# Performance work log

Hardware: AMD Instinct MI355X
Metric: run time of the kernel (lower is better)

## Reference

```python
import jax, jax.numpy as jnp
import numpy as np

N = 50000
E = 800000
HIDDEN = 128
NUM_HEADS = 8
D_HEAD = HIDDEN // NUM_HEADS


def setup_inputs() -> dict:
    key = jax.random.key(0)
    ks = jax.random.split(key, 12)
    sc = 1.0 / np.sqrt(HIDDEN)
    inp = {
        "h": jax.random.normal(ks[0], (N, HIDDEN), dtype=jnp.float32),
        "rows": jax.random.randint(ks[1], (E,), 0, N, dtype=jnp.int32),
        "cols": jax.random.randint(ks[2], (E,), 0, N, dtype=jnp.int32),
        "Wq": jax.random.normal(ks[3], (HIDDEN, HIDDEN), dtype=jnp.float32) * sc,
        "bq": jax.random.normal(ks[4], (HIDDEN,), dtype=jnp.float32) * sc,
        "Wk": jax.random.normal(ks[5], (HIDDEN, HIDDEN), dtype=jnp.float32) * sc,
        "bk": jax.random.normal(ks[6], (HIDDEN,), dtype=jnp.float32) * sc,
        "Wv": jax.random.normal(ks[7], (HIDDEN, HIDDEN), dtype=jnp.float32) * sc,
        "bv": jax.random.normal(ks[8], (HIDDEN,), dtype=jnp.float32) * sc,
        "Wo": jax.random.normal(ks[9], (HIDDEN, HIDDEN), dtype=jnp.float32) * sc,
        "bo": jax.random.normal(ks[10], (HIDDEN,), dtype=jnp.float32) * sc,
    }
    return inp


def reference(h, rows, cols, Wq, bq, Wk, bk, Wv, bv, Wo, bo):
    n = h.shape[0]
    scaling = D_HEAD ** (-0.5)
    # projections; torch-style reshape splits hidden as (d_head, num_heads)
    q = ((h @ Wq.T + bq).reshape(n, D_HEAD, NUM_HEADS)) * scaling
    k = (h @ Wk.T + bk).reshape(n, D_HEAD, NUM_HEADS)
    v = (h @ Wv.T + bv).reshape(n, D_HEAD, NUM_HEADS)
    # SDDMM: per-edge, per-head score = q[row] . k[col]   -> [E, H]
    scores = jnp.einsum("edh,edh->eh", q[rows], k[cols])
    # row-wise (destination) stable softmax over variable-degree neighborhoods
    m = jax.ops.segment_max(scores, rows, num_segments=n)  # [N, H]
    e = jnp.exp(scores - m[rows])
    s = jax.ops.segment_sum(e, rows, num_segments=n)  # [N, H]
    attn = e / s[rows]  # [E, H]
    # SpMM: out[i] = sum_{(i,j) in E} attn[e] * v[j]
    out = jax.ops.segment_sum(attn[:, None, :] * v[cols], rows, num_segments=n)
    return out.reshape(n, HIDDEN) @ Wo.T + bo
```

## Files before the change

kernel.cpp:

```cpp
#include <hip/hip_runtime.h>
#include <math.h>

#define N_NODES 50000
#define N_EDGES 800000
#define HID 128
#define CAP 64

#define SCAT_TH   (N_EDGES / 8)
#define SCAT_BLK  ((SCAT_TH + 255) / 256)
#define WCVT_BLK  64
#define HCVT_BLK  (N_NODES * HID / 4 / 256)
#define PREP_BLK  (SCAT_BLK + WCVT_BLK + HCVT_BLK)

#define QKV_BX    ((N_NODES + 31) / 32)
#define ATTN_BLK  ((N_NODES + 3) / 4)
#define OUT_BLK   ((N_NODES + 63) / 64)

typedef _Float16 f16_t;
typedef f16_t f16x8 __attribute__((ext_vector_type(8)));
typedef f16_t f16x2 __attribute__((ext_vector_type(2)));
typedef float f32x4 __attribute__((ext_vector_type(4)));

__device__ __forceinline__ ushort f2h_bits(float x) {
    union { f16_t h; ushort u; } c; c.h = (f16_t)x; return c.u;
}
__device__ __forceinline__ f16x2 as_h2(uint u) {
    union { uint u_; f16x2 h; } c; c.u_ = u; return c.h;
}

__global__ __launch_bounds__(256) void prep(
    const float* __restrict__ h,
    const float* __restrict__ Wq, const float* __restrict__ Wk,
    const float* __restrict__ Wv, const float* __restrict__ Wo,
    ushort* __restrict__ hf, ushort* __restrict__ wf,
    const int* __restrict__ rows, const int* __restrict__ cols,
    int* __restrict__ cnt, ushort* __restrict__ slots)
{
    const int b = blockIdx.x;
    const int tid = threadIdx.x;

    if (b < SCAT_BLK) {
        const int t = b * 256 + tid;
        if (t < SCAT_TH) {
            const int4* r4 = (const int4*)rows + (size_t)t * 2;
            const int4* c4 = (const int4*)cols + (size_t)t * 2;
            int4 ra = r4[0], rb2 = r4[1];
            int4 ca = c4[0], cb = c4[1];
            const int r[8] = {ra.x, ra.y, ra.z, ra.w, rb2.x, rb2.y, rb2.z, rb2.w};
            const int c[8] = {ca.x, ca.y, ca.z, ca.w, cb.x, cb.y, cb.z, cb.w};
            int p[8];
#pragma unroll
            for (int u = 0; u < 8; ++u)
                p[u] = atomicAdd(&cnt[r[u] << 4], 1);
#pragma unroll
            for (int u = 0; u < 8; ++u)
                if (p[u] < CAP) slots[(size_t)r[u] * CAP + p[u]] = (ushort)c[u];
        }
    } else if (b < SCAT_BLK + WCVT_BLK) {
        const int t = (b - SCAT_BLK) * 256 + tid;
        const int m = t >> 12, i = t & 4095;
        const float* src = (m == 0) ? Wq : (m == 1) ? Wk : (m == 2) ? Wv : Wo;
        float4 f = ((const float4*)src)[i];
        ushort4 o;
        o.x = f2h_bits(f.x); o.y = f2h_bits(f.y);
        o.z = f2h_bits(f.z); o.w = f2h_bits(f.w);
        ((ushort4*)(wf + m * 16384))[i] = o;
    } else {
        const int t = (b - SCAT_BLK - WCVT_BLK) * 256 + tid;
        float4 f = ((const float4*)h)[t];
        ushort4 o;
        o.x = f2h_bits(f.x); o.y = f2h_bits(f.y);
        o.z = f2h_bits(f.z); o.w = f2h_bits(f.w);
        ((ushort4*)hf)[t] = o;
    }
}

__global__ __launch_bounds__(256) void gemm_qkv(
    const ushort* __restrict__ hf, const ushort* __restrict__ wf,
    const float* __restrict__ bq, const float* __restrict__ bk,
    const float* __restrict__ bv,
    uint* __restrict__ qp, uint2* __restrict__ kv)
{
    const int lane = threadIdx.x & 63;
    const int wid  = threadIdx.x >> 6;
    const int mrow = lane & 15;
    const int quad = lane >> 4;
    const int rb   = blockIdx.x * 32;
    const int T    = blockIdx.y * 4 + wid;
    const int c    = T * 16 + mrow;

    f16x8 a[2][4];
#pragma unroll
    for (int s = 0; s < 2; ++s) {
        int ar = rb + s * 16 + mrow;
        if (ar >= N_NODES) ar = N_NODES - 1;
        const ushort* ap = hf + (size_t)ar * HID + quad * 8;
#pragma unroll
        for (int kc = 0; kc < 4; ++kc) a[s][kc] = *(const f16x8*)(ap + kc * 32);
    }
    f16x8 bQ[4], bK[4], bV[4];
#pragma unroll
    for (int kc = 0; kc < 4; ++kc) {
        const int off = c * HID + kc * 32 + quad * 8;
        bQ[kc] = *(const f16x8*)(wf + off);
        bK[kc] = *(const f16x8*)(wf + 16384 + off);
        bV[kc] = *(const f16x8*)(wf + 32768 + off);
    }

    f32x4 aq[2], ak[2], av[2];
#pragma unroll
    for (int s = 0; s < 2; ++s) {
        aq[s] = (f32x4){0.f, 0.f, 0.f, 0.f};
        ak[s] = (f32x4){0.f, 0.f, 0.f, 0.f};
        av[s] = (f32x4){0.f, 0.f, 0.f, 0.f};
    }
#pragma unroll
    for (int s = 0; s < 2; ++s)
#pragma unroll
        for (int kc = 0; kc < 4; ++kc) {
            aq[s] = __builtin_amdgcn_mfma_f32_16x16x32_f16(a[s][kc], bQ[kc], aq[s], 0, 0, 0);
            ak[s] = __builtin_amdgcn_mfma_f32_16x16x32_f16(a[s][kc], bK[kc], ak[s], 0, 0, 0);
            av[s] = __builtin_amdgcn_mfma_f32_16x16x32_f16(a[s][kc], bV[kc], av[s], 0, 0, 0);
        }

    const float bqc = bq[c], bkc = bk[c], bvc = bv[c];
    const bool  lo  = (mrow & 8) == 0;
    const int   i   = mrow & 7;
#pragma unroll
    for (int s = 0; s < 2; ++s)
#pragma unroll
        for (int r = 0; r < 4; ++r) {
            const int orow = rb + s * 16 + quad * 4 + r;
            uint qv = f2h_bits((aq[s][r] + bqc) * 0.25f);
            uint kb = f2h_bits(ak[s][r] + bkc);
            uint vb = f2h_bits(av[s][r] + bvc);
            uint qh = __shfl_xor((int)qv, 8);
            uint kh = __shfl_xor((int)kb, 8);
            uint vh = __shfl_xor((int)vb, 8);
            if (lo && orow < N_NODES) {
                const size_t base = (size_t)orow * 64 + 8 * T + i;
                qp[base] = qv | (qh << 16);
                kv[base] = make_uint2(kb | (kh << 16), vb | (vh << 16));
            }
        }
}

__device__ __forceinline__ void edge_acc(uint2 rr, f16x2 qh,
                                         float& l, float& Oa, float& Ob)
{
    float p = __builtin_amdgcn_fdot2(as_h2(rr.x), qh, 0.f, false);
    p += __shfl_xor(p, 8);
    p += __shfl_xor(p, 16);
    p += __shfl_xor(p, 32);
    float ex = __expf(p);
    f16x2 vh = as_h2(rr.y);
    l  += ex;
    Oa += ex * (float)vh[0];
    Ob += ex * (float)vh[1];
}

__global__ __launch_bounds__(256) void attn(
    const uint* __restrict__ qp, const uint2* __restrict__ kv,
    const int* __restrict__ cnt, const ushort* __restrict__ slots,
    ushort* __restrict__ ao)
{
    const int lane = threadIdx.x & 63;
    const int node = blockIdx.x * 4 + (threadIdx.x >> 6);
    if (node >= N_NODES) return;

    const f16x2 qh = as_h2(qp[(size_t)node * 64 + lane]);

    int deg = cnt[node << 4];
    if (deg > CAP) deg = CAP;
    const int myslot = (lane < deg) ? (int)slots[(size_t)node * CAP + lane] : 0;

    float ls[4] = {0.f, 0.f, 0.f, 0.f};
    float Oa[4] = {0.f, 0.f, 0.f, 0.f};
    float Ob[4] = {0.f, 0.f, 0.f, 0.f};

    int j = 0;
    for (; j + 4 <= deg; j += 4) {
        int s0 = __shfl(myslot, j);
        int s1 = __shfl(myslot, j + 1);
        int s2 = __shfl(myslot, j + 2);
        int s3 = __shfl(myslot, j + 3);
        uint2 r0 = kv[(size_t)s0 * 64 + lane];
        uint2 r1 = kv[(size_t)s1 * 64 + lane];
        uint2 r2 = kv[(size_t)s2 * 64 + lane];
        uint2 r3 = kv[(size_t)s3 * 64 + lane];
        edge_acc(r0, qh, ls[0], Oa[0], Ob[0]);
        edge_acc(r1, qh, ls[1], Oa[1], Ob[1]);
        edge_acc(r2, qh, ls[2], Oa[2], Ob[2]);
        edge_acc(r3, qh, ls[3], Oa[3], Ob[3]);
    }
    for (; j < deg; ++j) {
        int s = __shfl(myslot, j);
        uint2 rr = kv[(size_t)s * 64 + lane];
        edge_acc(rr, qh, ls[0], Oa[0], Ob[0]);
    }

    const float l  = (ls[0] + ls[1]) + (ls[2] + ls[3]);
    const float O0 = (Oa[0] + Oa[1]) + (Oa[2] + Oa[3]);
    const float O1 = (Ob[0] + Ob[1]) + (Ob[2] + Ob[3]);
    const float inv = (l > 0.f) ? 1.f / l : 0.f;

    const int ce = 16 * (lane >> 3) + (lane & 7);
    ao[(size_t)node * HID + ce]     = f2h_bits(O0 * inv);
    ao[(size_t)node * HID + ce + 8] = f2h_bits(O1 * inv);
}

__global__ __launch_bounds__(256) void gemm_out(
    const ushort* __restrict__ A, const ushort* __restrict__ wfo,
    const float* __restrict__ bias, float* __restrict__ out)
{
    const int lane = threadIdx.x & 63;
    const int wid  = threadIdx.x >> 6;
    const int mrow = lane & 15;
    const int quad = lane >> 4;
    const int rb   = blockIdx.x * 64;

    const int c0 = wid * 32 + mrow;
    const int c1 = c0 + 16;

    f16x8 a[4][4];
#pragma unroll
    for (int s = 0; s < 4; ++s) {
        int ar = rb + s * 16 + mrow;
        if (ar >= N_NODES) ar = N_NODES - 1;
        const ushort* ap = A + (size_t)ar * HID + quad * 8;
#pragma unroll
        for (int kc = 0; kc < 4; ++kc) a[s][kc] = *(const f16x8*)(ap + kc * 32);
    }
    f16x8 b0[4], b1[4];
#pragma unroll
    for (int kc = 0; kc < 4; ++kc) {
        b0[kc] = *(const f16x8*)(wfo + c0 * HID + kc * 32 + quad * 8);
        b1[kc] = *(const f16x8*)(wfo + c1 * HID + kc * 32 + quad * 8);
    }

    f32x4 acc[4][2];
#pragma unroll
    for (int s = 0; s < 4; ++s) {
        acc[s][0] = (f32x4){0.f, 0.f, 0.f, 0.f};
        acc[s][1] = (f32x4){0.f, 0.f, 0.f, 0.f};
    }
#pragma unroll
    for (int s = 0; s < 4; ++s)
#pragma unroll
        for (int kc = 0; kc < 4; ++kc) {
            acc[s][0] = __builtin_amdgcn_mfma_f32_16x16x32_f16(a[s][kc], b0[kc], acc[s][0], 0, 0, 0);
            acc[s][1] = __builtin_amdgcn_mfma_f32_16x16x32_f16(a[s][kc], b1[kc], acc[s][1], 0, 0, 0);
        }

    const float bc0 = bias[c0], bc1 = bias[c1];
#pragma unroll
    for (int s = 0; s < 4; ++s)
#pragma unroll
        for (int r = 0; r < 4; ++r) {
            const int orow = rb + s * 16 + quad * 4 + r;
            if (orow < N_NODES) {
                out[(size_t)orow * HID + c0] = acc[s][0][r] + bc0;
                out[(size_t)orow * HID + c1] = acc[s][1][r] + bc1;
            }
        }
}

extern "C" void kernel_launch(void* const* d_in, const int* in_sizes, int n_in,
                              void* d_out, int out_size, void* d_ws, size_t ws_size,
                              hipStream_t stream)
{
    const float* h    = (const float*)d_in[0];
    const int*   rows = (const int*)  d_in[1];
    const int*   cols = (const int*)  d_in[2];
    const float* Wq   = (const float*)d_in[3];
    const float* bq   = (const float*)d_in[4];
    const float* Wk   = (const float*)d_in[5];
    const float* bk   = (const float*)d_in[6];
    const float* Wv   = (const float*)d_in[7];
    const float* bv   = (const float*)d_in[8];
    const float* Wo   = (const float*)d_in[9];
    const float* bo   = (const float*)d_in[10];
    float* out = (float*)d_out;

    char* ws = (char*)d_ws;
    uint*   qp    = (uint*)ws;    ws += (size_t)N_NODES * 64 * 4;
    uint2*  kv    = (uint2*)ws;   ws += (size_t)N_NODES * 64 * 8;
    ushort* hf    = (ushort*)ws;  ws += (size_t)N_NODES * HID * 2;
    ushort* ao    = (ushort*)ws;  ws += (size_t)N_NODES * HID * 2;
    ushort* wf    = (ushort*)ws;  ws += 4 * 16384 * 2;
    int*    cnt   = (int*)ws;     ws += (size_t)N_NODES * 64;
    ushort* slots = (ushort*)ws;

    hipMemsetAsync(cnt, 0, (size_t)N_NODES * 64, stream);

    dim3 blk(256);
    prep<<<PREP_BLK, blk, 0, stream>>>(h, Wq, Wk, Wv, Wo, hf, wf,
                                       rows, cols, cnt, slots);
    gemm_qkv<<<dim3(QKV_BX, 2), blk, 0, stream>>>(hf, wf, bq, bk, bv, qp, kv);
    attn<<<ATTN_BLK, blk, 0, stream>>>(qp, kv, cnt, slots, ao);
    gemm_out<<<OUT_BLK, blk, 0, stream>>>(ao, wf + 3 * 16384, bo, out);
}
```

Baseline: 235.3 us.

## Regroup QKV output by head and process eight edges per wavefront in attention

Permutes the Q/K/V projection output columns so each head's 16 dims are contiguous, and permutes Wo's input columns to match the new attention output layout. The attention kernel now assigns 8 lanes per head and 8 edges per step, so each lane computes a full head dot product locally with fdot2 and 64-byte vector loads. This removes the per-edge cross-lane shuffle reductions. It adds a 16-register accumulator per lane, a final butterfly reduction over edge groups, and masked work on partial edge groups.

```diff
diff --git a/kernel.cpp b/kernel.cpp
--- a/kernel.cpp
+++ b/kernel.cpp
@@ -61,10 +61,21 @@
         const int m = t >> 12, i = t & 4095;
         const float* src = (m == 0) ? Wq : (m == 1) ? Wk : (m == 2) ? Wv : Wo;
         float4 f = ((const float4*)src)[i];
-        ushort4 o;
-        o.x = f2h_bits(f.x); o.y = f2h_bits(f.y);
-        o.z = f2h_bits(f.z); o.w = f2h_bits(f.w);
-        ((ushort4*)(wf + m * 16384))[i] = o;
+        if (m < 3) {
+            ushort4 o;
+            o.x = f2h_bits(f.x); o.y = f2h_bits(f.y);
+            o.z = f2h_bits(f.z); o.w = f2h_bits(f.w);
+            ((ushort4*)(wf + m * 16384))[i] = o;
+        } else {
+            const int c  = i >> 5;
+            const int k0 = (i & 31) * 4;
+            const int d  = k0 >> 3;
+            ushort* wo = wf + 3 * 16384 + c * HID + d;
+            wo[((k0 + 0) & 7) << 4] = f2h_bits(f.x);
+            wo[((k0 + 1) & 7) << 4] = f2h_bits(f.y);
+            wo[((k0 + 2) & 7) << 4] = f2h_bits(f.z);
+            wo[((k0 + 3) & 7) << 4] = f2h_bits(f.w);
+        }
     } else {
         const int t = (b - SCAT_BLK - WCVT_BLK) * 256 + tid;
         float4 f = ((const float4*)h)[t];
@@ -87,7 +98,7 @@
     const int quad = lane >> 4;
     const int rb   = blockIdx.x * 32;
     const int T    = blockIdx.y * 4 + wid;
-    const int c    = T * 16 + mrow;
+    const int c    = ((mrow & 7) << 4) + ((mrow >> 3) << 3) + T;
 
     f16x8 a[2][4];
 #pragma unroll
@@ -145,20 +156,6 @@
         }
 }
 
-__device__ __forceinline__ void edge_acc(uint2 rr, f16x2 qh,
-                                         float& l, float& Oa, float& Ob)
-{
-    float p = __builtin_amdgcn_fdot2(as_h2(rr.x), qh, 0.f, false);
-    p += __shfl_xor(p, 8);
-    p += __shfl_xor(p, 16);
-    p += __shfl_xor(p, 32);
-    float ex = __expf(p);
-    f16x2 vh = as_h2(rr.y);
-    l  += ex;
-    Oa += ex * (float)vh[0];
-    Ob += ex * (float)vh[1];
-}
-
 __global__ __launch_bounds__(256) void attn(
     const uint* __restrict__ qp, const uint2* __restrict__ kv,
     const int* __restrict__ cnt, const ushort* __restrict__ slots,
@@ -167,46 +164,70 @@
     const int lane = threadIdx.x & 63;
     const int node = blockIdx.x * 4 + (threadIdx.x >> 6);
     if (node >= N_NODES) return;
-
-    const f16x2 qh = as_h2(qp[(size_t)node * 64 + lane]);
+    const int es = lane >> 3;
+    const int h  = lane & 7;
+
+    const uint4* qb = (const uint4*)(qp + (size_t)node * 64 + h * 8);
+    const uint4 q0 = qb[0], q1 = qb[1];
 
     int deg = cnt[node << 4];
     if (deg > CAP) deg = CAP;
     const int myslot = (lane < deg) ? (int)slots[(size_t)node * CAP + lane] : 0;
 
-    float ls[4] = {0.f, 0.f, 0.f, 0.f};
-    float Oa[4] = {0.f, 0.f, 0.f, 0.f};
-    float Ob[4] = {0.f, 0.f, 0.f, 0.f};
-
-    int j = 0;
-    for (; j + 4 <= deg; j += 4) {
-        int s0 = __shfl(myslot, j);
-        int s1 = __shfl(myslot, j + 1);
-        int s2 = __shfl(myslot, j + 2);
-        int s3 = __shfl(myslot, j + 3);
-        uint2 r0 = kv[(size_t)s0 * 64 + lane];
-        uint2 r1 = kv[(size_t)s1 * 64 + lane];
-        uint2 r2 = kv[(size_t)s2 * 64 + lane];
-        uint2 r3 = kv[(size_t)s3 * 64 + lane];
-        edge_acc(r0, qh, ls[0], Oa[0], Ob[0]);
-        edge_acc(r1, qh, ls[1], Oa[1], Ob[1]);
-        edge_acc(r2, qh, ls[2], Oa[2], Ob[2]);
-        edge_acc(r3, qh, ls[3], Oa[3], Ob[3]);
-    }
-    for (; j < deg; ++j) {
-        int s = __shfl(myslot, j);
-        uint2 rr = kv[(size_t)s * 64 + lane];
-        edge_acc(rr, qh, ls[0], Oa[0], Ob[0]);
-    }
-
-    const float l  = (ls[0] + ls[1]) + (ls[2] + ls[3]);
-    const float O0 = (Oa[0] + Oa[1]) + (Oa[2] + Oa[3]);
-    const float O1 = (Ob[0] + Ob[1]) + (Ob[2] + Ob[3]);
+    float l = 0.f;
+    float O[16];
+#pragma unroll
+    for (int d = 0; d < 16; ++d) O[d] = 0.f;
+
+    for (int j = 0; j < deg; j += 8) {
+        const int sl = __shfl(myslot, j + es);
+        const uint4* kp = (const uint4*)(kv + (size_t)sl * 64 + h * 8);
+        const uint4 r0 = kp[0], r1 = kp[1], r2 = kp[2], r3 = kp[3];
+        float s;
+        s = __builtin_amdgcn_fdot2(as_h2(r0.x), as_h2(q0.x), 0.f, false);
+        s = __builtin_amdgcn_fdot2(as_h2(r0.z), as_h2(q0.y), s, false);
+        s = __builtin_amdgcn_fdot2(as_h2(r1.x), as_h2(q0.z), s, false);
+        s = __builtin_amdgcn_fdot2(as_h2(r1.z), as_h2(q0.w), s, false);
+        s = __builtin_amdgcn_fdot2(as_h2(r2.x), as_h2(q1.x), s, false);
+        s = __builtin_amdgcn_fdot2(as_h2(r2.z), as_h2(q1.y), s, false);
+        s = __builtin_amdgcn_fdot2(as_h2(r3.x), as_h2(q1.z), s, false);
+        s = __builtin_amdgcn_fdot2(as_h2(r3.z), as_h2(q1.w), s, false);
+        const float ex = ((j + es) < deg) ? __expf(s) : 0.f;
+        l += ex;
+        f16x2 v;
+        v = as_h2(r0.y); O[0]  += ex * (float)v[0]; O[1]  += ex * (float)v[1];
+        v = as_h2(r0.w); O[2]  += ex * (float)v[0]; O[3]  += ex * (float)v[1];
+        v = as_h2(r1.y); O[4]  += ex * (float)v[0]; O[5]  += ex * (float)v[1];
+        v = as_h2(r1.w); O[6]  += ex * (float)v[0]; O[7]  += ex * (float)v[1];
+        v = as_h2(r2.y); O[8]  += ex * (float)v[0]; O[9]  += ex * (float)v[1];
+        v = as_h2(r2.w); O[10] += ex * (float)v[0]; O[11] += ex * (float)v[1];
+        v = as_h2(r3.y); O[12] += ex * (float)v[0]; O[13] += ex * (float)v[1];
+        v = as_h2(r3.w); O[14] += ex * (float)v[0]; O[15] += ex * (float)v[1];
+    }
+
+#pragma unroll
+    for (int m = 8; m <= 32; m <<= 1) {
+        l += __shfl_xor(l, m);
+#pragma unroll
+        for (int d = 0; d < 16; ++d) O[d] += __shfl_xor(O[d], m);
+    }
     const float inv = (l > 0.f) ? 1.f / l : 0.f;
 
-    const int ce = 16 * (lane >> 3) + (lane & 7);
-    ao[(size_t)node * HID + ce]     = f2h_bits(O0 * inv);
-    ao[(size_t)node * HID + ce + 8] = f2h_bits(O1 * inv);
+    if (es == 0) {
+        uint4 st;
+        st.x = (uint)f2h_bits(O[0] * inv) | ((uint)f2h_bits(O[1] * inv) << 16);
+        st.y = (uint)f2h_bits(O[2] * inv) | ((uint)f2h_bits(O[3] * inv) << 16);
+        st.z = (uint)f2h_bits(O[4] * inv) | ((uint)f2h_bits(O[5] * inv) << 16);
+        st.w = (uint)f2h_bits(O[6] * inv) | ((uint)f2h_bits(O[7] * inv) << 16);
+        *(uint4*)(ao + (size_t)node * HID + h * 16) = st;
+    } else if (es == 1) {
+        uint4 st;
+        st.x = (uint)f2h_bits(O[8]  * inv) | ((uint)f2h_bits(O[9]  * inv) << 16);
+        st.y = (uint)f2h_bits(O[10] * inv) | ((uint)f2h_bits(O[11] * inv) << 16);
+        st.z = (uint)f2h_bits(O[12] * inv) | ((uint)f2h_bits(O[13] * inv) << 16);
+        st.w = (uint)f2h_bits(O[14] * inv) | ((uint)f2h_bits(O[15] * inv) << 16);
+        *(uint4*)(ao + (size_t)node * HID + h * 16 + 8) = st;
+    }
 }
 
 __global__ __launch_bounds__(256) void gemm_out(
```

Result: slower. 378.8 us (+61.0%).
